# Optimization experiments

Measured on AMD Instinct MI355X. Metric: run time of the kernel, lower is better.

## Reference

```python
import jax, jax.numpy as jnp
import numpy as np
from math import sqrt

ALPHA = 1.0
EPS = 1e-8


def setup_inputs() -> dict:
    key = jax.random.key(0)
    k1, k2, k3 = jax.random.split(key, 3)
    B, L, S, H, E = 4, 2048, 2048, 16, 64
    queries = jax.random.normal(k1, (B, L, H, E), dtype=jnp.float32)
    keys = jax.random.normal(k2, (B, S, H, E), dtype=jnp.float32)
    values = jax.random.normal(k3, (B, S, H, E), dtype=jnp.float32)
    return {"queries": queries, "keys": keys, "values": values}


def reference(queries, keys, values):
    B, L, H, E = queries.shape
    scale = 1.0 / sqrt(E)
    # dot product scores: [B,H,L,S]
    dot = jnp.einsum('blhe,bshe->bhls', queries, keys)
    # squared norms: [B,H,L,1] and [B,H,1,S]
    qn2 = jnp.sum(queries * queries, axis=-1).transpose(0, 2, 1)[..., :, None]
    kn2 = jnp.sum(keys * keys, axis=-1).transpose(0, 2, 1)[..., None, :]
    # wedge (parallelogram area) norm^2 = |q|^2|k|^2 - (q.k)^2, clipped at 0
    wedge_norm = jnp.sqrt(jax.nn.relu(qn2 * kn2 - dot * dot) + EPS)
    scores = ((1.0 - ALPHA) * dot + ALPHA * wedge_norm) * scale
    A = jax.nn.softmax(scores, axis=-1)  # no mask (mask_flag=False), dropout=0
    V = jnp.einsum('bhls,bshd->blhd', A, values)
    return V, jnp.mean(jnp.abs(scores))
```

## Files before the change

### kernel.cpp

```cpp
#include <hip/hip_runtime.h>
#include <math.h>

constexpr int Bb = 4, Ll = 2048, Ss = 2048, Hh = 16, Ee = 64;
constexpr float S2E  = 0.125f * 1.44269504088896341f;
constexpr float EPS2 = 1e-8f * S2E * S2E;
constexpr float INV_CNT = 1.0f / (4.0f * 16.0f * 2048.0f * 2048.0f);
constexpr float SUM_SCALE = INV_CNT * 0.69314718055994531f;

typedef __attribute__((ext_vector_type(8)))  short short8;
typedef __attribute__((ext_vector_type(4)))  float floatx4;
typedef __attribute__((ext_vector_type(16))) float floatx16;

#define MFMA32 __builtin_amdgcn_mfma_f32_32x32x16_bf16

#define GLL(gp, lp_)                                                       \
  __builtin_amdgcn_global_load_lds(                                        \
      (const __attribute__((address_space(1))) unsigned int*)(gp),         \
      (__attribute__((address_space(3))) unsigned int*)(lp_), 16, 0, 0)

__device__ __forceinline__ unsigned bfrnd(float f) {
  unsigned u = __builtin_bit_cast(unsigned, f);
  return u + 0x7fffu + ((u >> 16) & 1u);
}
__device__ __forceinline__ float sq4(float4 v) {
  return v.x * v.x + v.y * v.y + v.z * v.z + v.w * v.w;
}
__device__ __forceinline__ float4 mul4(float4 v, float s) {
  float4 r; r.x = v.x * s; r.y = v.y * s; r.z = v.z * s; r.w = v.w * s;
  return r;
}
__device__ __forceinline__ short8 pack8(float4 x, float4 y) {
  union { short8 s; unsigned u[4]; } r;
  r.u[0] = __builtin_amdgcn_perm(bfrnd(x.y), bfrnd(x.x), 0x07060302u);
  r.u[1] = __builtin_amdgcn_perm(bfrnd(x.w), bfrnd(x.z), 0x07060302u);
  r.u[2] = __builtin_amdgcn_perm(bfrnd(y.y), bfrnd(y.x), 0x07060302u);
  r.u[3] = __builtin_amdgcn_perm(bfrnd(y.w), bfrnd(y.z), 0x07060302u);
  return r.s;
}
__device__ __forceinline__ void pl32swap(unsigned &a, unsigned &b) {
  asm("v_permlane32_swap_b32 %0, %1" : "+v"(a), "+v"(b));
}

__global__ __launch_bounds__(256) void geom_pre_kernel(
    const float* __restrict__ Kg, const float* __restrict__ Vg,
    short* __restrict__ Kbf, short* __restrict__ Vtg,
    float* __restrict__ kn2g, float* __restrict__ sumg) {
  const int tid = threadIdx.x, bid = blockIdx.x;
  const int st = bid & 31, h = (bid >> 5) & 15, b = bid >> 9;
  const int s0 = st * 64, bh = b * 16 + h;
  if (bid == 0 && tid == 0) *sumg = 0.0f;

  const int r64 = tid >> 2, ec = (tid & 3) * 16;
  const float4* kp = (const float4*)(Kg + (((size_t)b * Ss + s0 + r64) * Hh + h) * Ee + ec);
  float4 k0 = kp[0], k1 = kp[1], k2 = kp[2], k3 = kp[3];
  float kn = sq4(k0) + sq4(k1) + sq4(k2) + sq4(k3);
  kn += __shfl_xor(kn, 1);
  kn += __shfl_xor(kn, 2);
  if ((tid & 3) == 0) kn2g[(size_t)bh * Ss + s0 + r64] = kn;
  short* ko = Kbf + ((size_t)bh * Ss + s0 + r64) * Ee + ec;
  *(short8*)(ko)     = pack8(k0, k1);
  *(short8*)(ko + 8) = pack8(k2, k3);

  const int sq = tid >> 4, eq = tid & 15;
  const float* vb = Vg + (((size_t)b * Ss + s0 + sq * 4) * Hh + h) * Ee + eq * 4;
  float4 r0 = *(const float4*)(vb);
  float4 r1 = *(const float4*)(vb + Hh * Ee);
  float4 r2 = *(const float4*)(vb + 2 * Hh * Ee);
  float4 r3 = *(const float4*)(vb + 3 * Hh * Ee);
  short* vo = Vtg + ((size_t)bh * Ee + eq * 4) * Ss + s0 + sq * 4;
#pragma unroll
  for (int j = 0; j < 4; ++j) {
    uint2 t;
    t.x = __builtin_amdgcn_perm(bfrnd((&r1.x)[j]), bfrnd((&r0.x)[j]), 0x07060302u);
    t.y = __builtin_amdgcn_perm(bfrnd((&r3.x)[j]), bfrnd((&r2.x)[j]), 0x07060302u);
    *(uint2*)(vo + (size_t)j * Ss) = t;
  }
}

constexpr int KB0 = 0, VB0 = 8192, KN2 = 16384;

__global__ __launch_bounds__(256, 4) void geom_attn_kernel(
    const float* __restrict__ Qg, const short* __restrict__ Kbf,
    const short* __restrict__ Vtg, const float* __restrict__ kn2g,
    float* __restrict__ outg, float* __restrict__ sumg) {
  __shared__ __align__(16) char smem[24576];

  const int tid = threadIdx.x, w = tid >> 6, lane = tid & 63;
  const int l31 = lane & 31, hi = lane >> 5;
  const int bid = blockIdx.x;
  const int lt = bid & 15, h = (bid >> 4) & 15, b = bid >> 8;
  const int bh = b * 16 + h;
  const int l0w = lt * 128 + w * 32;

  short8 qB[4];
  float qn2v;
  {
    const float* qrow = Qg + (((size_t)b * Ll + l0w + l31) * Hh + h) * Ee;
    float qn = 0.f;
#pragma unroll
    for (int ks = 0; ks < 4; ++ks) {
      float4 a0 = mul4(*(const float4*)(qrow + ks * 16 + hi * 8), S2E);
      float4 a1 = mul4(*(const float4*)(qrow + ks * 16 + hi * 8 + 4), S2E);
      qn += sq4(a0) + sq4(a1);
      qB[ks] = pack8(a0, a1);
    }
    qn += __shfl_xor(qn, 32);
    qn2v = qn;
  }

  const int rK = tid >> 3, pK = tid & 7;
  const char* kSrc = (const char*)Kbf + (size_t)bh * (Ss * 128) + rK * 128 + ((pK ^ (rK & 7)) * 16);
  const int eV = tid >> 2;
  const char* vSrc = (const char*)Vtg + (size_t)bh * (Ss * 128) + eV * (Ss * 2) + (((tid & 3) ^ (eV & 3)) * 16);
  char* kDstW = smem + KB0 + w * 1024;
  char* vDstW = smem + VB0 + w * 1024;

  {
    const char* knSrc = (const char*)kn2g + (size_t)bh * 8192 + (size_t)tid * 16;
    GLL(knSrc, smem + KN2 + w * 1024);
    GLL(knSrc + 4096, smem + KN2 + w * 1024 + 4096);
  }

  GLL(kSrc, kDstW);
  GLL(vSrc, vDstW);
  kSrc += 4096;
  vSrc += 64;

  floatx16 o[2] = {};
  float lp = 0.f, scsum = 0.f;

  const int kSwz = l31 & 7;
  const int vSwz = l31 & 3;

  for (int it = 0; it < 64; ++it) {
    const int p = it & 1;
    __syncthreads();
    GLL(kSrc, kDstW + (p ^ 1) * 4096);
    GLL(vSrc, vDstW + (p ^ 1) * 4096);
    kSrc += 4096;
    vSrc += 64;

    const char* Kb = smem + KB0 + p * 4096;
    const char* Vb = smem + VB0 + p * 4096;

    short8 ka0 = *(const short8*)(Kb + l31 * 128 + (((0 + hi) ^ kSwz) * 16));
    short8 ka1 = *(const short8*)(Kb + l31 * 128 + (((2 + hi) ^ kSwz) * 16));
    short8 ka2 = *(const short8*)(Kb + l31 * 128 + (((4 + hi) ^ kSwz) * 16));
    short8 ka3 = *(const short8*)(Kb + l31 * 128 + (((6 + hi) ^ kSwz) * 16));
    floatx16 d = {};
    d = MFMA32(ka0, qB[0], d, 0, 0, 0);
    d = MFMA32(ka1, qB[1], d, 0, 0, 0);
    d = MFMA32(ka2, qB[2], d, 0, 0, 0);
    d = MFMA32(ka3, qB[3], d, 0, 0, 0);

    short8 vb00 = *(const short8*)(Vb + l31 * 64 + (((0 + hi) ^ vSwz) * 16));
    short8 vb01 = *(const short8*)(Vb + l31 * 64 + (((2 + hi) ^ vSwz) * 16));
    short8 vb10 = *(const short8*)(Vb + (32 + l31) * 64 + (((0 + hi) ^ vSwz) * 16));
    short8 vb11 = *(const short8*)(Vb + (32 + l31) * 64 + (((2 + hi) ^ vSwz) * 16));

    float4 knv0 = *(const float4*)(smem + KN2 + it * 128 + 0 * 32 + hi * 16);
    float4 knv1 = *(const float4*)(smem + KN2 + it * 128 + 1 * 32 + hi * 16);
    float4 knv2 = *(const float4*)(smem + KN2 + it * 128 + 2 * 32 + hi * 16);
    float4 knv3 = *(const float4*)(smem + KN2 + it * 128 + 3 * 32 + hi * 16);

    unsigned pk[4][2];
#pragma unroll
    for (int q = 0; q < 4; ++q) {
      const float4 knq = (q == 0) ? knv0 : (q == 1) ? knv1 : (q == 2) ? knv2 : knv3;
      float pe[4];
#pragma unroll
      for (int r = 0; r < 4; ++r) {
        float dot = d[4 * q + r];
        float w2 = fmaf(-dot, dot, qn2v * (&knq.x)[r]);
        w2 = fmaxf(w2, EPS2);
        float rt = __builtin_amdgcn_sqrtf(w2);
        scsum += rt;
        float e = __builtin_amdgcn_exp2f(rt);
        lp += e;
        pe[r] = e;
      }
      pk[q][0] = __builtin_amdgcn_perm(__builtin_bit_cast(unsigned, pe[1]),
                                       __builtin_bit_cast(unsigned, pe[0]), 0x07060302u);
      pk[q][1] = __builtin_amdgcn_perm(__builtin_bit_cast(unsigned, pe[3]),
                                       __builtin_bit_cast(unsigned, pe[2]), 0x07060302u);
    }

    pl32swap(pk[0][0], pk[1][0]);
    pl32swap(pk[0][1], pk[1][1]);
    pl32swap(pk[2][0], pk[3][0]);
    pl32swap(pk[2][1], pk[3][1]);
    union { unsigned u[4]; short8 s; } pa0, pa1;
    pa0.u[0] = pk[0][0]; pa0.u[1] = pk[0][1]; pa0.u[2] = pk[1][0]; pa0.u[3] = pk[1][1];
    pa1.u[0] = pk[2][0]; pa1.u[1] = pk[2][1]; pa1.u[2] = pk[3][0]; pa1.u[3] = pk[3][1];

    o[0] = MFMA32(pa0.s, vb00, o[0], 0, 0, 0);
    o[0] = MFMA32(pa1.s, vb01, o[0], 0, 0, 0);
    o[1] = MFMA32(pa0.s, vb10, o[1], 0, 0, 0);
    o[1] = MFMA32(pa1.s, vb11, o[1], 0, 0, 0);
  }

  __syncthreads();

  lp += __shfl_xor(lp, 32);
  float lpinv = 1.0f / lp;

#pragma unroll
  for (int r = 0; r < 16; ++r) {
    const int row = (r & 3) + 8 * (r >> 2) + 4 * hi;
    float inv = __shfl(lpinv, row);
    float* orow = outg + (((size_t)b * Ll + l0w + row) * Hh + h) * Ee + l31;
    orow[0]  = o[0][r] * inv;
    orow[32] = o[1][r] * inv;
  }

  scsum += __shfl_xor(scsum, 1);
  scsum += __shfl_xor(scsum, 2);
  scsum += __shfl_xor(scsum, 4);
  scsum += __shfl_xor(scsum, 8);
  scsum += __shfl_xor(scsum, 16);
  scsum += __shfl_xor(scsum, 32);
  if (lane == 0) atomicAdd(sumg, scsum * SUM_SCALE);
}

extern "C" void kernel_launch(void* const* d_in, const int* in_sizes, int n_in,
                              void* d_out, int out_size, void* d_ws, size_t ws_size,
                              hipStream_t stream) {
  const float* Q = (const float*)d_in[0];
  const float* K = (const float*)d_in[1];
  const float* V = (const float*)d_in[2];
  float* out   = (float*)d_out;
  float* sumsc = out + (size_t)Bb * Ll * Hh * Ee;

  short* Kbf = (short*)d_ws;
  short* Vtg = Kbf + (size_t)Bb * Hh * Ss * Ee;
  float* kn2 = (float*)(Vtg + (size_t)Bb * Hh * Ee * Ss);

  hipLaunchKernelGGL(geom_pre_kernel, dim3(Bb * Hh * (Ss / 64)), dim3(256), 0,
                     stream, K, V, Kbf, Vtg, kn2, sumsc);
  hipLaunchKernelGGL(geom_attn_kernel, dim3(Bb * Hh * (Ll / 128)), dim3(256), 0,
                     stream, Q, Kbf, Vtg, kn2, out, sumsc);
}
```

Baseline: 259.3 us.

## Triple-buffer K/V loads, transpose V via LDS, swizzle block order, add setprio

The attention loop moves from double to triple buffering. It uses explicit vmcnt waits and a bare barrier, so each prefetch runs two iterations ahead. The block index is remapped to interleave blocks across heads and batches. s_setprio raises wave priority around the MFMA groups, and the score and exp accumulations are tree-reduced. The preprocessing kernel transposes V through padded LDS so the global stores are coalesced 16-byte writes. The cost is more LDS per block, which may reduce occupancy, and more fragile manual wait-count handling.

After: 253.3 us. 2.3% less time.

```diff
diff --git a/kernel.cpp b/kernel.cpp
--- a/kernel.cpp
+++ b/kernel.cpp
@@ -45,6 +45,7 @@
     const float* __restrict__ Kg, const float* __restrict__ Vg,
     short* __restrict__ Kbf, short* __restrict__ Vtg,
     float* __restrict__ kn2g, float* __restrict__ sumg) {
+  __shared__ __align__(16) short vsm[64 * 66];
   const int tid = threadIdx.x, bid = blockIdx.x;
   const int st = bid & 31, h = (bid >> 5) & 15, b = bid >> 9;
   const int s0 = st * 64, bh = b * 16 + h;
@@ -67,28 +68,40 @@
   float4 r1 = *(const float4*)(vb + Hh * Ee);
   float4 r2 = *(const float4*)(vb + 2 * Hh * Ee);
   float4 r3 = *(const float4*)(vb + 3 * Hh * Ee);
-  short* vo = Vtg + ((size_t)bh * Ee + eq * 4) * Ss + s0 + sq * 4;
 #pragma unroll
   for (int j = 0; j < 4; ++j) {
-    uint2 t;
-    t.x = __builtin_amdgcn_perm(bfrnd((&r1.x)[j]), bfrnd((&r0.x)[j]), 0x07060302u);
-    t.y = __builtin_amdgcn_perm(bfrnd((&r3.x)[j]), bfrnd((&r2.x)[j]), 0x07060302u);
-    *(uint2*)(vo + (size_t)j * Ss) = t;
-  }
-}
-
-constexpr int KB0 = 0, VB0 = 8192, KN2 = 16384;
+    unsigned lo = __builtin_amdgcn_perm(bfrnd((&r1.x)[j]), bfrnd((&r0.x)[j]), 0x07060302u);
+    unsigned hh = __builtin_amdgcn_perm(bfrnd((&r3.x)[j]), bfrnd((&r2.x)[j]), 0x07060302u);
+    short* row = vsm + (eq * 4 + j) * 66 + sq * 4;
+    *(unsigned*)(row)     = lo;
+    *(unsigned*)(row + 2) = hh;
+  }
+  __syncthreads();
+  const int e = tid >> 2, sc = (tid & 3) * 16;
+  const short* rr = vsm + e * 66 + sc;
+  uint4 a, c;
+  a.x = *(const unsigned*)(rr + 0);  a.y = *(const unsigned*)(rr + 2);
+  a.z = *(const unsigned*)(rr + 4);  a.w = *(const unsigned*)(rr + 6);
+  c.x = *(const unsigned*)(rr + 8);  c.y = *(const unsigned*)(rr + 10);
+  c.z = *(const unsigned*)(rr + 12); c.w = *(const unsigned*)(rr + 14);
+  short* vo = Vtg + ((size_t)bh * Ee + e) * Ss + s0 + sc;
+  *(uint4*)(vo)     = a;
+  *(uint4*)(vo + 8) = c;
+}
+
+constexpr int KB0 = 0, VB0 = 12288, KN2 = 24576;
 
 __global__ __launch_bounds__(256, 4) void geom_attn_kernel(
     const float* __restrict__ Qg, const short* __restrict__ Kbf,
     const short* __restrict__ Vtg, const float* __restrict__ kn2g,
     float* __restrict__ outg, float* __restrict__ sumg) {
-  __shared__ __align__(16) char smem[24576];
+  __shared__ __align__(16) char smem[32768];
 
   const int tid = threadIdx.x, w = tid >> 6, lane = tid & 63;
   const int l31 = lane & 31, hi = lane >> 5;
   const int bid = blockIdx.x;
-  const int lt = bid & 15, h = (bid >> 4) & 15, b = bid >> 8;
+  const int wk = ((bid & 7) << 7) | (bid >> 3);
+  const int lt = wk & 15, h = (wk >> 4) & 15, b = wk >> 8;
   const int bh = b * 16 + h;
   const int l0w = lt * 128 + w * 32;
 
@@ -123,8 +136,10 @@
 
   GLL(kSrc, kDstW);
   GLL(vSrc, vDstW);
-  kSrc += 4096;
-  vSrc += 64;
+  kSrc += 4096; vSrc += 64;
+  GLL(kSrc, kDstW + 4096);
+  GLL(vSrc, vDstW + 4096);
+  kSrc += 4096; vSrc += 64;
 
   floatx16 o[2] = {};
   float lp = 0.f, scsum = 0.f;
@@ -132,26 +147,34 @@
   const int kSwz = l31 & 7;
   const int vSwz = l31 & 3;
 
+  int pb = 0;
   for (int it = 0; it < 64; ++it) {
-    const int p = it & 1;
-    __syncthreads();
-    GLL(kSrc, kDstW + (p ^ 1) * 4096);
-    GLL(vSrc, vDstW + (p ^ 1) * 4096);
-    kSrc += 4096;
-    vSrc += 64;
-
-    const char* Kb = smem + KB0 + p * 4096;
-    const char* Vb = smem + VB0 + p * 4096;
+    if (it == 63) asm volatile("s_waitcnt vmcnt(0)" ::: "memory");
+    else          asm volatile("s_waitcnt vmcnt(2)" ::: "memory");
+    __builtin_amdgcn_s_barrier();
+    asm volatile("" ::: "memory");
+
+    if (it < 62) {
+      const int pf = pb ? pb - 1 : 2;
+      GLL(kSrc, kDstW + pf * 4096);
+      GLL(vSrc, vDstW + pf * 4096);
+      kSrc += 4096; vSrc += 64;
+    }
+
+    const char* Kb = smem + KB0 + pb * 4096;
+    const char* Vb = smem + VB0 + pb * 4096;
 
     short8 ka0 = *(const short8*)(Kb + l31 * 128 + (((0 + hi) ^ kSwz) * 16));
     short8 ka1 = *(const short8*)(Kb + l31 * 128 + (((2 + hi) ^ kSwz) * 16));
     short8 ka2 = *(const short8*)(Kb + l31 * 128 + (((4 + hi) ^ kSwz) * 16));
     short8 ka3 = *(const short8*)(Kb + l31 * 128 + (((6 + hi) ^ kSwz) * 16));
+    __builtin_amdgcn_s_setprio(1);
     floatx16 d = {};
     d = MFMA32(ka0, qB[0], d, 0, 0, 0);
     d = MFMA32(ka1, qB[1], d, 0, 0, 0);
     d = MFMA32(ka2, qB[2], d, 0, 0, 0);
     d = MFMA32(ka3, qB[3], d, 0, 0, 0);
+    __builtin_amdgcn_s_setprio(0);
 
     short8 vb00 = *(const short8*)(Vb + l31 * 64 + (((0 + hi) ^ vSwz) * 16));
     short8 vb01 = *(const short8*)(Vb + l31 * 64 + (((2 + hi) ^ vSwz) * 16));
@@ -167,18 +190,17 @@
 #pragma unroll
     for (int q = 0; q < 4; ++q) {
       const float4 knq = (q == 0) ? knv0 : (q == 1) ? knv1 : (q == 2) ? knv2 : knv3;
-      float pe[4];
+      float pe[4], rt4[4];
 #pragma unroll
       for (int r = 0; r < 4; ++r) {
         float dot = d[4 * q + r];
         float w2 = fmaf(-dot, dot, qn2v * (&knq.x)[r]);
         w2 = fmaxf(w2, EPS2);
-        float rt = __builtin_amdgcn_sqrtf(w2);
-        scsum += rt;
-        float e = __builtin_amdgcn_exp2f(rt);
-        lp += e;
-        pe[r] = e;
+        rt4[r] = __builtin_amdgcn_sqrtf(w2);
+        pe[r]  = __builtin_amdgcn_exp2f(rt4[r]);
       }
+      scsum += (rt4[0] + rt4[1]) + (rt4[2] + rt4[3]);
+      lp    += (pe[0] + pe[1]) + (pe[2] + pe[3]);
       pk[q][0] = __builtin_amdgcn_perm(__builtin_bit_cast(unsigned, pe[1]),
                                        __builtin_bit_cast(unsigned, pe[0]), 0x07060302u);
       pk[q][1] = __builtin_amdgcn_perm(__builtin_bit_cast(unsigned, pe[3]),
@@ -193,10 +215,14 @@
     pa0.u[0] = pk[0][0]; pa0.u[1] = pk[0][1]; pa0.u[2] = pk[1][0]; pa0.u[3] = pk[1][1];
     pa1.u[0] = pk[2][0]; pa1.u[1] = pk[2][1]; pa1.u[2] = pk[3][0]; pa1.u[3] = pk[3][1];
 
+    __builtin_amdgcn_s_setprio(1);
     o[0] = MFMA32(pa0.s, vb00, o[0], 0, 0, 0);
     o[0] = MFMA32(pa1.s, vb01, o[0], 0, 0, 0);
     o[1] = MFMA32(pa0.s, vb10, o[1], 0, 0, 0);
     o[1] = MFMA32(pa1.s, vb11, o[1], 0, 0, 0);
+    __builtin_amdgcn_s_setprio(0);
+
+    pb = (pb == 2) ? 0 : pb + 1;
   }
 
   __syncthreads();
```
